# Kernel optimization log

Hardware: AMD Instinct MI355X
Metric: run time of the kernel (lower is better)

The kernel has to match this reference:

```python
import jax, jax.numpy as jnp
import numpy as np

DIM = 1024
NUM_HEADS = 16
HEAD_DIM = DIM // NUM_HEADS
SCALE = HEAD_DIM ** -0.5
CAUSAL = True


def setup_inputs() -> dict:
    key = jax.random.key(0)
    k_x, k_qkv, k_proj, k_pb = jax.random.split(key, 4)
    B, S = 4, 2048
    x = jax.random.normal(k_x, (B, S, DIM), dtype=jnp.float32)
    # nn.Linear(dim, 3*dim, bias=False): weight [3*dim, dim]; store transposed [dim, 3*dim]
    w_qkv = jax.random.normal(k_qkv, (DIM, 3 * DIM), dtype=jnp.float32) * (DIM ** -0.5)
    w_proj = jax.random.normal(k_proj, (DIM, DIM), dtype=jnp.float32) * (DIM ** -0.5)
    b_proj = jax.random.normal(k_pb, (DIM,), dtype=jnp.float32) * 0.01
    return {"x": x, "w_qkv": w_qkv, "w_proj": w_proj, "b_proj": b_proj}


def reference(x, w_qkv, w_proj, b_proj):
    B, S, C = x.shape
    # qkv: [B, S, 3, H, D] -> q,k,v each [B, H, S, D]
    qkv = (x @ w_qkv).reshape(B, S, 3, NUM_HEADS, HEAD_DIM)
    qkv = jnp.transpose(qkv, (2, 0, 3, 1, 4))
    q, k, v = qkv[0], qkv[1], qkv[2]
    # scores [B, H, S, S]
    attn = jnp.einsum('bhqd,bhkd->bhqk', q, k) * SCALE
    if CAUSAL:
        causal_mask = jnp.triu(jnp.ones((S, S), dtype=bool), k=1)
        attn = jnp.where(causal_mask, -jnp.inf, attn)
    attn = jax.nn.softmax(attn, axis=-1)
    out = jnp.einsum('bhqk,bhkd->bhqd', attn, v)
    out = jnp.transpose(out, (0, 2, 1, 3)).reshape(B, S, C)
    return out @ w_proj + b_proj
```

## Files before the change

kernel.cpp:

```cpp
#include <hip/hip_runtime.h>
#include <hip/hip_bf16.h>
#include <math.h>

#define DIMC 1024
#define NHEADS 16
#define HDIM 64
#define BATCH 4
#define SEQ 2048
#define NROWS (BATCH * SEQ)
#define ATTN_SCALE 0.125f
#define LOG2E 1.4426950408889634f

typedef __attribute__((ext_vector_type(8))) short short8;
typedef __attribute__((ext_vector_type(4))) short short4v;
typedef __attribute__((ext_vector_type(4))) float f32x4;

static __device__ __forceinline__ short f2bf(float f) {
    __hip_bfloat16 h = __float2bfloat16(f);
    return *reinterpret_cast<short*>(&h);
}

static __device__ __forceinline__ void gload16(const void* g, void* l) {
    __builtin_amdgcn_global_load_lds(
        (const __attribute__((address_space(1))) unsigned int*)g,
        (__attribute__((address_space(3))) unsigned int*)l, 16, 0, 0);
}

__global__ __launch_bounds__(256)
void xcvt(const float* __restrict__ in, unsigned short* __restrict__ out) {
    int i = blockIdx.x * 256 + threadIdx.x;
    const float4* p = reinterpret_cast<const float4*>(in) + 2 * i;
    float4 a = p[0], b = p[1];
    short8 pk;
    pk[0] = f2bf(a.x); pk[1] = f2bf(a.y); pk[2] = f2bf(a.z); pk[3] = f2bf(a.w);
    pk[4] = f2bf(b.x); pk[5] = f2bf(b.y); pk[6] = f2bf(b.z); pk[7] = f2bf(b.w);
    reinterpret_cast<short8*>(out)[i] = pk;
}

__global__ __launch_bounds__(256)
void transpose_cvt(const float* __restrict__ src, unsigned short* __restrict__ dst,
                   int N) {
    __shared__ float t[64][65];
    const int tid = threadIdx.x;
    const int cb = blockIdx.x * 64;
    const int rb = blockIdx.y * 64;
#pragma unroll
    for (int e = 0; e < 4; e++) {
        int idx = tid + e * 256;
        int row = idx >> 4;
        int c4 = (idx & 15) << 2;
        *reinterpret_cast<float4*>(&t[row][c4]) =
            *reinterpret_cast<const float4*>(&src[(size_t)(rb + row) * N + cb + c4]);
    }
    __syncthreads();
#pragma unroll
    for (int e = 0; e < 2; e++) {
        int idx = tid + e * 256;
        int col = idx >> 3;
        int k8 = (idx & 7) << 3;
        short8 pk;
#pragma unroll
        for (int j = 0; j < 8; j++) pk[j] = f2bf(t[k8 + j][col]);
        *reinterpret_cast<short8*>(&dst[(size_t)(cb + col) * 1024 + rb + k8]) = pk;
    }
}

__global__ __launch_bounds__(256)
void qkv_gemm_mfma(const unsigned short* __restrict__ Xbf,
                   const unsigned short* __restrict__ Wt,
                   unsigned short* __restrict__ qo, unsigned short* __restrict__ ko,
                   unsigned short* __restrict__ vt) {
    __shared__ short Alds[128][32];
    __shared__ short Blds[128][32];
    const int tid = threadIdx.x;
    const int lane = tid & 63;
    const int wave = tid >> 6;
    const int wr = wave >> 1, wc = wave & 1;
    const int rowbase = blockIdx.y * 128;
    const int colbase = blockIdx.x * 128;
    const int g = lane >> 4, li = lane & 15;
    const int srow0 = (wave * 2 + 0) * 16 + (lane >> 2);
    const int srow1 = (wave * 2 + 1) * 16 + (lane >> 2);
    const int scol = (lane & 3) * 8;
    short* aflat = &Alds[0][0];
    short* bflat = &Blds[0][0];

    f32x4 acc[4][4];
#pragma unroll
    for (int m = 0; m < 4; m++)
#pragma unroll
        for (int n = 0; n < 4; n++) acc[m][n] = (f32x4){0.f, 0.f, 0.f, 0.f};

    for (int k0 = 0; k0 < DIMC; k0 += 32) {
        gload16(&Xbf[(size_t)(rowbase + srow0) * DIMC + k0 + scol],
                aflat + (wave * 2 + 0) * 512);
        gload16(&Xbf[(size_t)(rowbase + srow1) * DIMC + k0 + scol],
                aflat + (wave * 2 + 1) * 512);
        gload16(&Wt[(size_t)(colbase + srow0) * 1024 + k0 + scol],
                bflat + (wave * 2 + 0) * 512);
        gload16(&Wt[(size_t)(colbase + srow1) * 1024 + k0 + scol],
                bflat + (wave * 2 + 1) * 512);
        __syncthreads();
        short8 af[4], bfr[4];
#pragma unroll
        for (int m = 0; m < 4; m++)
            af[m] = *reinterpret_cast<const short8*>(&Alds[wr * 64 + m * 16 + li][g * 8]);
#pragma unroll
        for (int n = 0; n < 4; n++)
            bfr[n] = *reinterpret_cast<const short8*>(&Blds[wc * 64 + n * 16 + li][g * 8]);
#pragma unroll
        for (int m = 0; m < 4; m++)
#pragma unroll
            for (int n = 0; n < 4; n++)
                acc[m][n] = __builtin_amdgcn_mfma_f32_16x16x32_bf16(
                    af[m], bfr[n], acc[m][n], 0, 0, 0);
        __syncthreads();
    }

    const int col0 = colbase + wc * 64;
    const int three = col0 >> 10;
    const int h = (col0 & 1023) >> 6;
    if (three < 2) {
        unsigned short* dst = (three == 0) ? qo : ko;
        const float mult = (three == 0) ? (ATTN_SCALE * LOG2E) : 1.0f;
#pragma unroll
        for (int n = 0; n < 4; n++) {
            int d = n * 16 + li;
#pragma unroll
            for (int m = 0; m < 4; m++) {
                int r0 = rowbase + wr * 64 + m * 16 + g * 4;
                int b = r0 >> 11;
                size_t base = ((size_t)(b * NHEADS + h) * SEQ) * HDIM + d;
#pragma unroll
                for (int r = 0; r < 4; r++) {
                    int s = (r0 + r) & 2047;
                    dst[base + (size_t)s * HDIM] = (unsigned short)f2bf(acc[m][n][r] * mult);
                }
            }
        }
    } else {
#pragma unroll
        for (int n = 0; n < 4; n++) {
            int d = n * 16 + li;
#pragma unroll
            for (int m = 0; m < 4; m++) {
                int r0 = rowbase + wr * 64 + m * 16 + g * 4;
                int b = r0 >> 11, s0 = r0 & 2047;
                short4v pk;
#pragma unroll
                for (int r = 0; r < 4; r++) pk[r] = f2bf(acc[m][n][r]);
                *reinterpret_cast<short4v*>(
                    &vt[((size_t)(b * NHEADS + h) * HDIM + d) * SEQ + s0]) = pk;
            }
        }
    }
}

__global__ __launch_bounds__(256)
void proj_gemm_mfma(const unsigned short* __restrict__ Abf,
                    const unsigned short* __restrict__ Wt,
                    const float* __restrict__ bias, float* __restrict__ out) {
    __shared__ short Alds[128][32];
    __shared__ short Blds[128][32];
    const int tid = threadIdx.x;
    const int lane = tid & 63;
    const int wave = tid >> 6;
    const int wr = wave >> 1, wc = wave & 1;
    const int rowbase = blockIdx.y * 128;
    const int colbase = blockIdx.x * 128;
    const int g = lane >> 4, li = lane & 15;
    const int srow0 = (wave * 2 + 0) * 16 + (lane >> 2);
    const int srow1 = (wave * 2 + 1) * 16 + (lane >> 2);
    const int scol = (lane & 3) * 8;
    short* aflat = &Alds[0][0];
    short* bflat = &Blds[0][0];

    f32x4 acc[4][4];
#pragma unroll
    for (int m = 0; m < 4; m++)
#pragma unroll
        for (int n = 0; n < 4; n++) acc[m][n] = (f32x4){0.f, 0.f, 0.f, 0.f};

    for (int k0 = 0; k0 < DIMC; k0 += 32) {
        gload16(&Abf[(size_t)(rowbase + srow0) * DIMC + k0 + scol],
                aflat + (wave * 2 + 0) * 512);
        gload16(&Abf[(size_t)(rowbase + srow1) * DIMC + k0 + scol],
                aflat + (wave * 2 + 1) * 512);
        gload16(&Wt[(size_t)(colbase + srow0) * 1024 + k0 + scol],
                bflat + (wave * 2 + 0) * 512);
        gload16(&Wt[(size_t)(colbase + srow1) * 1024 + k0 + scol],
                bflat + (wave * 2 + 1) * 512);
        __syncthreads();
        short8 af[4], bfr[4];
#pragma unroll
        for (int m = 0; m < 4; m++)
            af[m] = *reinterpret_cast<const short8*>(&Alds[wr * 64 + m * 16 + li][g * 8]);
#pragma unroll
        for (int n = 0; n < 4; n++)
            bfr[n] = *reinterpret_cast<const short8*>(&Blds[wc * 64 + n * 16 + li][g * 8]);
#pragma unroll
        for (int m = 0; m < 4; m++)
#pragma unroll
            for (int n = 0; n < 4; n++)
                acc[m][n] = __builtin_amdgcn_mfma_f32_16x16x32_bf16(
                    af[m], bfr[n], acc[m][n], 0, 0, 0);
        __syncthreads();
    }

#pragma unroll
    for (int n = 0; n < 4; n++) {
        int col = colbase + wc * 64 + n * 16 + li;
        float bv = bias[col];
#pragma unroll
        for (int m = 0; m < 4; m++) {
            int r0 = rowbase + wr * 64 + m * 16 + g * 4;
#pragma unroll
            for (int r = 0; r < 4; r++)
                out[(size_t)(r0 + r) * DIMC + col] = acc[m][n][r] + bv;
        }
    }
}

__global__ __launch_bounds__(256)
void flash_attn_mfma(const unsigned short* __restrict__ qg,
                     const unsigned short* __restrict__ kg,
                     const unsigned short* __restrict__ vt,
                     unsigned short* __restrict__ og) {
    __shared__ short Klds[2][64][64];
    __shared__ short Vlds[2][64][64];
    __shared__ short Plds[4][32][64];
    const int tid = threadIdx.x;
    const int lane = tid & 63;
    const int w = tid >> 6;
    const int g = lane >> 4, li = lane & 15;
    const int sw = li & 7;
    const int orig = blockIdx.x;
    const int swz = (orig & 7) * 128 + (orig >> 3);
    const int bh = swz >> 4;
    const int qtile = 15 - (swz & 15);
    const size_t head = (size_t)bh * SEQ * HDIM;
    const int b = bh >> 4, h = bh & 15;

    const int c0r = tid >> 3, c0c = tid & 7;

    const int qbase = qtile * 128;
    const int qw = qbase + w * 32;
    const int nt = 2 * qtile + 2;

    short8 bq[2][2];
#pragma unroll
    for (int n = 0; n < 2; n++)
#pragma unroll
        for (int ds = 0; ds < 2; ds++)
            bq[n][ds] = *reinterpret_cast<const short8*>(
                &qg[head + (size_t)(qw + li + 16 * n) * HDIM + ds * 32 + g * 8]);

    f32x4 accO[4][2];
#pragma unroll
    for (int df = 0; df < 4; df++)
#pragma unroll
        for (int n = 0; n < 2; n++) accO[df][n] = (f32x4){0.f, 0.f, 0.f, 0.f};
    float mrow[2] = {-INFINITY, -INFINITY};
    float lrow[2] = {0.f, 0.f};

    const unsigned short* kp = kg + head + (size_t)c0r * HDIM + c0c * 8;
    const unsigned short* vp = vt + head + (size_t)c0r * SEQ + c0c * 8;

    short8 kreg0, kreg1, vreg0, vreg1;
    kreg0 = *reinterpret_cast<const short8*>(kp);
    kreg1 = *reinterpret_cast<const short8*>(kp + 32 * HDIM);
    vreg0 = *reinterpret_cast<const short8*>(vp);
    vreg1 = *reinterpret_cast<const short8*>(vp + 32 * SEQ);
    kp += 64 * HDIM; vp += 64;
    {
        const int sw0 = (c0c ^ (c0r & 7)) * 8;
        const int sw1 = (c0c ^ ((c0r + 32) & 7)) * 8;
        *reinterpret_cast<short8*>(&Klds[0][c0r][sw0]) = kreg0;
        *reinterpret_cast<short8*>(&Vlds[0][c0r][sw0]) = vreg0;
        *reinterpret_cast<short8*>(&Klds[0][c0r + 32][sw1]) = kreg1;
        *reinterpret_cast<short8*>(&Vlds[0][c0r + 32][sw1]) = vreg1;
    }
    __syncthreads();

    for (int t = 0; t < nt; t++) {
        const int kvbase = t * 64;
        const int buf = t & 1;
        const bool more = (t + 1 < nt);
        if (more) {
            kreg0 = *reinterpret_cast<const short8*>(kp);
            kreg1 = *reinterpret_cast<const short8*>(kp + 32 * HDIM);
            vreg0 = *reinterpret_cast<const short8*>(vp);
            vreg1 = *reinterpret_cast<const short8*>(vp + 32 * SEQ);
            kp += 64 * HDIM; vp += 64;
        }

        if (kvbase <= qw + 31) {
            f32x4 s[4][2];
#pragma unroll
            for (int m = 0; m < 4; m++)
#pragma unroll
                for (int n = 0; n < 2; n++) s[m][n] = (f32x4){0.f, 0.f, 0.f, 0.f};
#pragma unroll
            for (int ds = 0; ds < 2; ds++) {
                short8 ak[4];
#pragma unroll
                for (int m = 0; m < 4; m++)
                    ak[m] = *reinterpret_cast<const short8*>(
                        &Klds[buf][li + 16 * m][(((ds * 4 + g) ^ sw)) * 8]);
#pragma unroll
                for (int m = 0; m < 4; m++)
#pragma unroll
                    for (int n = 0; n < 2; n++)
                        s[m][n] = __builtin_amdgcn_mfma_f32_16x16x32_bf16(
                            ak[m], bq[n][ds], s[m][n], 0, 0, 0);
            }
            const bool diag = (kvbase + 63 > qw);
            if (diag) {
#pragma unroll
                for (int n = 0; n < 2; n++) {
                    int q = qw + li + 16 * n;
#pragma unroll
                    for (int m = 0; m < 4; m++)
#pragma unroll
                        for (int r = 0; r < 4; r++) {
                            int kv = kvbase + 16 * m + 4 * g + r;
                            if (kv > q) s[m][n][r] = -INFINITY;
                        }
                }
            }
            float corr[2];
#pragma unroll
            for (int n = 0; n < 2; n++) {
                float a0 = fmaxf(fmaxf(s[0][n][0], s[0][n][1]), fmaxf(s[0][n][2], s[0][n][3]));
                float a1 = fmaxf(fmaxf(s[1][n][0], s[1][n][1]), fmaxf(s[1][n][2], s[1][n][3]));
                float a2 = fmaxf(fmaxf(s[2][n][0], s[2][n][1]), fmaxf(s[2][n][2], s[2][n][3]));
                float a3 = fmaxf(fmaxf(s[3][n][0], s[3][n][1]), fmaxf(s[3][n][2], s[3][n][3]));
                float tm = fmaxf(fmaxf(a0, a1), fmaxf(a2, a3));
                tm = fmaxf(tm, __shfl_xor(tm, 16));
                tm = fmaxf(tm, __shfl_xor(tm, 32));
                float mnew = fmaxf(mrow[n], tm);
                corr[n] = __builtin_amdgcn_exp2f(mrow[n] - mnew);
                mrow[n] = mnew;
            }
            float sm[4][2];
#pragma unroll
            for (int m = 0; m < 4; m++) {
#pragma unroll
                for (int n = 0; n < 2; n++) {
                    float p0 = __builtin_amdgcn_exp2f(s[m][n][0] - mrow[n]);
                    float p1 = __builtin_amdgcn_exp2f(s[m][n][1] - mrow[n]);
                    float p2 = __builtin_amdgcn_exp2f(s[m][n][2] - mrow[n]);
                    float p3 = __builtin_amdgcn_exp2f(s[m][n][3] - mrow[n]);
                    sm[m][n] = (p0 + p1) + (p2 + p3);
                    unsigned u01 = (__float_as_uint(p1) & 0xFFFF0000u) |
                                   (__float_as_uint(p0) >> 16);
                    unsigned u23 = (__float_as_uint(p3) & 0xFFFF0000u) |
                                   (__float_as_uint(p2) >> 16);
                    *reinterpret_cast<uint2*>(
                        &Plds[w][li + 16 * n]
                             [((2 * m + (g >> 1)) ^ sw) * 8 + (g & 1) * 4]) =
                        make_uint2(u01, u23);
                }
            }
#pragma unroll
            for (int n = 0; n < 2; n++) {
                float ts = (sm[0][n] + sm[1][n]) + (sm[2][n] + sm[3][n]);
                ts += __shfl_xor(ts, 16);
                ts += __shfl_xor(ts, 32);
                lrow[n] = lrow[n] * corr[n] + ts;
            }
            bool nore = (corr[0] == 1.0f) && (corr[1] == 1.0f);
            if (!__all((int)nore)) {
#pragma unroll
                for (int df = 0; df < 4; df++)
#pragma unroll
                    for (int n = 0; n < 2; n++) {
                        accO[df][n][0] *= corr[n]; accO[df][n][1] *= corr[n];
                        accO[df][n][2] *= corr[n]; accO[df][n][3] *= corr[n];
                    }
            }
#pragma unroll
            for (int ks = 0; ks < 2; ks++) {
                short8 av[4], bp[2];
#pragma unroll
                for (int df = 0; df < 4; df++)
                    av[df] = *reinterpret_cast<const short8*>(
                        &Vlds[buf][li + 16 * df][((ks * 4 + g) ^ sw) * 8]);
#pragma unroll
                for (int n = 0; n < 2; n++)
                    bp[n] = *reinterpret_cast<const short8*>(
                        &Plds[w][li + 16 * n][((ks * 4 + g) ^ sw) * 8]);
#pragma unroll
                for (int df = 0; df < 4; df++)
#pragma unroll
                    for (int n = 0; n < 2; n++)
                        accO[df][n] = __builtin_amdgcn_mfma_f32_16x16x32_bf16(
                            av[df], bp[n], accO[df][n], 0, 0, 0);
            }
        }

        if (more) {
            const int nbuf = buf ^ 1;
            const int sw0 = (c0c ^ (c0r & 7)) * 8;
            const int sw1 = (c0c ^ ((c0r + 32) & 7)) * 8;
            *reinterpret_cast<short8*>(&Klds[nbuf][c0r][sw0]) = kreg0;
            *reinterpret_cast<short8*>(&Vlds[nbuf][c0r][sw0]) = vreg0;
            *reinterpret_cast<short8*>(&Klds[nbuf][c0r + 32][sw1]) = kreg1;
            *reinterpret_cast<short8*>(&Vlds[nbuf][c0r + 32][sw1]) = vreg1;
        }
        __syncthreads();
    }

#pragma unroll
    for (int n = 0; n < 2; n++) {
        float inv = 1.0f / lrow[n];
        int q = qw + li + 16 * n;
        size_t rowoff = (size_t)(b * SEQ + q) * DIMC + h * HDIM;
#pragma unroll
        for (int df = 0; df < 4; df++) {
            short4v pk;
#pragma unroll
            for (int r = 0; r < 4; r++) pk[r] = f2bf(accO[df][n][r] * inv);
            *reinterpret_cast<short4v*>(&og[rowoff + 16 * df + 4 * g]) = pk;
        }
    }
}

extern "C" void kernel_launch(void* const* d_in, const int* in_sizes, int n_in,
                              void* d_out, int out_size, void* d_ws, size_t ws_size,
                              hipStream_t stream) {
    const float* x      = (const float*)d_in[0];
    const float* w_qkv  = (const float*)d_in[1];
    const float* w_proj = (const float*)d_in[2];
    const float* b_proj = (const float*)d_in[3];
    float* out = (float*)d_out;

    char* w = (char*)d_ws;
    unsigned short* qb  = (unsigned short*)(w);
    unsigned short* kb  = (unsigned short*)(w + ((size_t)16 << 20));
    unsigned short* vtb = (unsigned short*)(w + ((size_t)32 << 20));
    unsigned short* ao  = (unsigned short*)(w + ((size_t)48 << 20));
    unsigned short* wqt = (unsigned short*)(w + ((size_t)64 << 20));
    unsigned short* wpt = (unsigned short*)(w + ((size_t)72 << 20));
    unsigned short* xbf = (unsigned short*)(w + ((size_t)80 << 20));

    xcvt<<<NROWS * DIMC / (256 * 8), 256, 0, stream>>>(x, xbf);
    transpose_cvt<<<dim3(3 * DIMC / 64, DIMC / 64), 256, 0, stream>>>(w_qkv, wqt, 3 * DIMC);
    transpose_cvt<<<dim3(DIMC / 64, DIMC / 64), 256, 0, stream>>>(w_proj, wpt, DIMC);
    qkv_gemm_mfma<<<dim3(3 * DIMC / 128, NROWS / 128), 256, 0, stream>>>(xbf, wqt, qb, kb, vtb);
    flash_attn_mfma<<<1024, 256, 0, stream>>>(qb, kb, vtb, ao);
    proj_gemm_mfma<<<dim3(DIMC / 128, NROWS / 128), 256, 0, stream>>>(ao, wpt, b_proj, out);
}
```

Measured before the change: 299.6 us.

## Pair causal q-tiles per attention block and double GEMM K-step to 64

The flash-attention kernel now launches half as many blocks, and each block handles two q-tiles (bx and 15-bx) of one head in sequence. This balances the causal triangular workload so every block does the same total number of KV tiles. Separately, both GEMMs load 64-wide K slices per iteration and issue two MFMA substeps per barrier pair, which halves the number of synchronizations. The cost is doubled LDS per GEMM block, and fewer attention blocks, which may reduce occupancy and latency hiding.

Measured after the change: 279.7 us. 1.07x faster.

```diff
diff --git a/kernel.cpp b/kernel.cpp
--- a/kernel.cpp
+++ b/kernel.cpp
@@ -70,8 +70,8 @@
                    const unsigned short* __restrict__ Wt,
                    unsigned short* __restrict__ qo, unsigned short* __restrict__ ko,
                    unsigned short* __restrict__ vt) {
-    __shared__ short Alds[128][32];
-    __shared__ short Blds[128][32];
+    __shared__ short Alds[128][64];
+    __shared__ short Blds[128][64];
     const int tid = threadIdx.x;
     const int lane = tid & 63;
     const int wave = tid >> 6;
@@ -79,9 +79,8 @@
     const int rowbase = blockIdx.y * 128;
     const int colbase = blockIdx.x * 128;
     const int g = lane >> 4, li = lane & 15;
-    const int srow0 = (wave * 2 + 0) * 16 + (lane >> 2);
-    const int srow1 = (wave * 2 + 1) * 16 + (lane >> 2);
-    const int scol = (lane & 3) * 8;
+    const int sr = lane >> 3;
+    const int sc = (lane & 7) * 8;
     short* aflat = &Alds[0][0];
     short* bflat = &Blds[0][0];
 
@@ -91,29 +90,34 @@
 #pragma unroll
         for (int n = 0; n < 4; n++) acc[m][n] = (f32x4){0.f, 0.f, 0.f, 0.f};
 
-    for (int k0 = 0; k0 < DIMC; k0 += 32) {
-        gload16(&Xbf[(size_t)(rowbase + srow0) * DIMC + k0 + scol],
-                aflat + (wave * 2 + 0) * 512);
-        gload16(&Xbf[(size_t)(rowbase + srow1) * DIMC + k0 + scol],
-                aflat + (wave * 2 + 1) * 512);
-        gload16(&Wt[(size_t)(colbase + srow0) * 1024 + k0 + scol],
-                bflat + (wave * 2 + 0) * 512);
-        gload16(&Wt[(size_t)(colbase + srow1) * 1024 + k0 + scol],
-                bflat + (wave * 2 + 1) * 512);
-        __syncthreads();
-        short8 af[4], bfr[4];
-#pragma unroll
-        for (int m = 0; m < 4; m++)
-            af[m] = *reinterpret_cast<const short8*>(&Alds[wr * 64 + m * 16 + li][g * 8]);
-#pragma unroll
-        for (int n = 0; n < 4; n++)
-            bfr[n] = *reinterpret_cast<const short8*>(&Blds[wc * 64 + n * 16 + li][g * 8]);
-#pragma unroll
-        for (int m = 0; m < 4; m++)
+    for (int k0 = 0; k0 < DIMC; k0 += 64) {
+#pragma unroll
+        for (int e = 0; e < 4; e++) {
+            int j = wave * 4 + e;
+            gload16(&Xbf[(size_t)(rowbase + j * 8 + sr) * DIMC + k0 + sc],
+                    aflat + j * 512);
+            gload16(&Wt[(size_t)(colbase + j * 8 + sr) * 1024 + k0 + sc],
+                    bflat + j * 512);
+        }
+        __syncthreads();
+#pragma unroll
+        for (int ks = 0; ks < 2; ks++) {
+            short8 af[4], bfr[4];
+#pragma unroll
+            for (int m = 0; m < 4; m++)
+                af[m] = *reinterpret_cast<const short8*>(
+                    &Alds[wr * 64 + m * 16 + li][ks * 32 + g * 8]);
 #pragma unroll
             for (int n = 0; n < 4; n++)
-                acc[m][n] = __builtin_amdgcn_mfma_f32_16x16x32_bf16(
-                    af[m], bfr[n], acc[m][n], 0, 0, 0);
+                bfr[n] = *reinterpret_cast<const short8*>(
+                    &Blds[wc * 64 + n * 16 + li][ks * 32 + g * 8]);
+#pragma unroll
+            for (int m = 0; m < 4; m++)
+#pragma unroll
+                for (int n = 0; n < 4; n++)
+                    acc[m][n] = __builtin_amdgcn_mfma_f32_16x16x32_bf16(
+                        af[m], bfr[n], acc[m][n], 0, 0, 0);
+        }
         __syncthreads();
     }
 
@@ -160,8 +164,8 @@
 void proj_gemm_mfma(const unsigned short* __restrict__ Abf,
                     const unsigned short* __restrict__ Wt,
                     const float* __restrict__ bias, float* __restrict__ out) {
-    __shared__ short Alds[128][32];
-    __shared__ short Blds[128][32];
+    __shared__ short Alds[128][64];
+    __shared__ short Blds[128][64];
     const int tid = threadIdx.x;
     const int lane = tid & 63;
     const int wave = tid >> 6;
@@ -169,9 +173,8 @@
     const int rowbase = blockIdx.y * 128;
     const int colbase = blockIdx.x * 128;
     const int g = lane >> 4, li = lane & 15;
-    const int srow0 = (wave * 2 + 0) * 16 + (lane >> 2);
-    const int srow1 = (wave * 2 + 1) * 16 + (lane >> 2);
-    const int scol = (lane & 3) * 8;
+    const int sr = lane >> 3;
+    const int sc = (lane & 7) * 8;
     short* aflat = &Alds[0][0];
     short* bflat = &Blds[0][0];
 
@@ -181,29 +184,34 @@
 #pragma unroll
         for (int n = 0; n < 4; n++) acc[m][n] = (f32x4){0.f, 0.f, 0.f, 0.f};
 
-    for (int k0 = 0; k0 < DIMC; k0 += 32) {
-        gload16(&Abf[(size_t)(rowbase + srow0) * DIMC + k0 + scol],
-                aflat + (wave * 2 + 0) * 512);
-        gload16(&Abf[(size_t)(rowbase + srow1) * DIMC + k0 + scol],
-                aflat + (wave * 2 + 1) * 512);
-        gload16(&Wt[(size_t)(colbase + srow0) * 1024 + k0 + scol],
-                bflat + (wave * 2 + 0) * 512);
-        gload16(&Wt[(size_t)(colbase + srow1) * 1024 + k0 + scol],
-                bflat + (wave * 2 + 1) * 512);
-        __syncthreads();
-        short8 af[4], bfr[4];
-#pragma unroll
-        for (int m = 0; m < 4; m++)
-            af[m] = *reinterpret_cast<const short8*>(&Alds[wr * 64 + m * 16 + li][g * 8]);
-#pragma unroll
-        for (int n = 0; n < 4; n++)
-            bfr[n] = *reinterpret_cast<const short8*>(&Blds[wc * 64 + n * 16 + li][g * 8]);
-#pragma unroll
-        for (int m = 0; m < 4; m++)
+    for (int k0 = 0; k0 < DIMC; k0 += 64) {
+#pragma unroll
+        for (int e = 0; e < 4; e++) {
+            int j = wave * 4 + e;
+            gload16(&Abf[(size_t)(rowbase + j * 8 + sr) * DIMC + k0 + sc],
+                    aflat + j * 512);
+            gload16(&Wt[(size_t)(colbase + j * 8 + sr) * 1024 + k0 + sc],
+                    bflat + j * 512);
+        }
+        __syncthreads();
+#pragma unroll
+        for (int ks = 0; ks < 2; ks++) {
+            short8 af[4], bfr[4];
+#pragma unroll
+            for (int m = 0; m < 4; m++)
+                af[m] = *reinterpret_cast<const short8*>(
+                    &Alds[wr * 64 + m * 16 + li][ks * 32 + g * 8]);
 #pragma unroll
             for (int n = 0; n < 4; n++)
-                acc[m][n] = __builtin_amdgcn_mfma_f32_16x16x32_bf16(
-                    af[m], bfr[n], acc[m][n], 0, 0, 0);
+                bfr[n] = *reinterpret_cast<const short8*>(
+                    &Blds[wc * 64 + n * 16 + li][ks * 32 + g * 8]);
+#pragma unroll
+            for (int m = 0; m < 4; m++)
+#pragma unroll
+                for (int n = 0; n < 4; n++)
+                    acc[m][n] = __builtin_amdgcn_mfma_f32_16x16x32_bf16(
+                        af[m], bfr[n], acc[m][n], 0, 0, 0);
+        }
         __syncthreads();
     }
 
@@ -235,194 +243,198 @@
     const int g = lane >> 4, li = lane & 15;
     const int sw = li & 7;
     const int orig = blockIdx.x;
-    const int swz = (orig & 7) * 128 + (orig >> 3);
-    const int bh = swz >> 4;
-    const int qtile = 15 - (swz & 15);
+    const int swz = (orig & 7) * 64 + (orig >> 3);
+    const int bx = swz & 7;
+    const int bh = swz >> 3;
     const size_t head = (size_t)bh * SEQ * HDIM;
     const int b = bh >> 4, h = bh & 15;
 
     const int c0r = tid >> 3, c0c = tid & 7;
 
-    const int qbase = qtile * 128;
-    const int qw = qbase + w * 32;
-    const int nt = 2 * qtile + 2;
-
-    short8 bq[2][2];
-#pragma unroll
-    for (int n = 0; n < 2; n++)
-#pragma unroll
-        for (int ds = 0; ds < 2; ds++)
-            bq[n][ds] = *reinterpret_cast<const short8*>(
-                &qg[head + (size_t)(qw + li + 16 * n) * HDIM + ds * 32 + g * 8]);
-
-    f32x4 accO[4][2];
-#pragma unroll
-    for (int df = 0; df < 4; df++)
-#pragma unroll
-        for (int n = 0; n < 2; n++) accO[df][n] = (f32x4){0.f, 0.f, 0.f, 0.f};
-    float mrow[2] = {-INFINITY, -INFINITY};
-    float lrow[2] = {0.f, 0.f};
-
-    const unsigned short* kp = kg + head + (size_t)c0r * HDIM + c0c * 8;
-    const unsigned short* vp = vt + head + (size_t)c0r * SEQ + c0c * 8;
-
-    short8 kreg0, kreg1, vreg0, vreg1;
-    kreg0 = *reinterpret_cast<const short8*>(kp);
-    kreg1 = *reinterpret_cast<const short8*>(kp + 32 * HDIM);
-    vreg0 = *reinterpret_cast<const short8*>(vp);
-    vreg1 = *reinterpret_cast<const short8*>(vp + 32 * SEQ);
-    kp += 64 * HDIM; vp += 64;
-    {
-        const int sw0 = (c0c ^ (c0r & 7)) * 8;
-        const int sw1 = (c0c ^ ((c0r + 32) & 7)) * 8;
-        *reinterpret_cast<short8*>(&Klds[0][c0r][sw0]) = kreg0;
-        *reinterpret_cast<short8*>(&Vlds[0][c0r][sw0]) = vreg0;
-        *reinterpret_cast<short8*>(&Klds[0][c0r + 32][sw1]) = kreg1;
-        *reinterpret_cast<short8*>(&Vlds[0][c0r + 32][sw1]) = vreg1;
-    }
-    __syncthreads();
-
-    for (int t = 0; t < nt; t++) {
-        const int kvbase = t * 64;
-        const int buf = t & 1;
-        const bool more = (t + 1 < nt);
-        if (more) {
-            kreg0 = *reinterpret_cast<const short8*>(kp);
-            kreg1 = *reinterpret_cast<const short8*>(kp + 32 * HDIM);
-            vreg0 = *reinterpret_cast<const short8*>(vp);
-            vreg1 = *reinterpret_cast<const short8*>(vp + 32 * SEQ);
-            kp += 64 * HDIM; vp += 64;
-        }
-
-        if (kvbase <= qw + 31) {
-            f32x4 s[4][2];
-#pragma unroll
-            for (int m = 0; m < 4; m++)
-#pragma unroll
-                for (int n = 0; n < 2; n++) s[m][n] = (f32x4){0.f, 0.f, 0.f, 0.f};
-#pragma unroll
-            for (int ds = 0; ds < 2; ds++) {
-                short8 ak[4];
-#pragma unroll
-                for (int m = 0; m < 4; m++)
-                    ak[m] = *reinterpret_cast<const short8*>(
-                        &Klds[buf][li + 16 * m][(((ds * 4 + g) ^ sw)) * 8]);
-#pragma unroll
-                for (int m = 0; m < 4; m++)
-#pragma unroll
-                    for (int n = 0; n < 2; n++)
-                        s[m][n] = __builtin_amdgcn_mfma_f32_16x16x32_bf16(
-                            ak[m], bq[n][ds], s[m][n], 0, 0, 0);
-            }
-            const bool diag = (kvbase + 63 > qw);
-            if (diag) {
-#pragma unroll
-                for (int n = 0; n < 2; n++) {
-                    int q = qw + li + 16 * n;
-#pragma unroll
-                    for (int m = 0; m < 4; m++)
-#pragma unroll
-                        for (int r = 0; r < 4; r++) {
-                            int kv = kvbase + 16 * m + 4 * g + r;
-                            if (kv > q) s[m][n][r] = -INFINITY;
-                        }
-                }
-            }
-            float corr[2];
-#pragma unroll
-            for (int n = 0; n < 2; n++) {
-                float a0 = fmaxf(fmaxf(s[0][n][0], s[0][n][1]), fmaxf(s[0][n][2], s[0][n][3]));
-                float a1 = fmaxf(fmaxf(s[1][n][0], s[1][n][1]), fmaxf(s[1][n][2], s[1][n][3]));
-                float a2 = fmaxf(fmaxf(s[2][n][0], s[2][n][1]), fmaxf(s[2][n][2], s[2][n][3]));
-                float a3 = fmaxf(fmaxf(s[3][n][0], s[3][n][1]), fmaxf(s[3][n][2], s[3][n][3]));
-                float tm = fmaxf(fmaxf(a0, a1), fmaxf(a2, a3));
-                tm = fmaxf(tm, __shfl_xor(tm, 16));
-                tm = fmaxf(tm, __shfl_xor(tm, 32));
-                float mnew = fmaxf(mrow[n], tm);
-                corr[n] = __builtin_amdgcn_exp2f(mrow[n] - mnew);
-                mrow[n] = mnew;
-            }
-            float sm[4][2];
-#pragma unroll
-            for (int m = 0; m < 4; m++) {
-#pragma unroll
-                for (int n = 0; n < 2; n++) {
-                    float p0 = __builtin_amdgcn_exp2f(s[m][n][0] - mrow[n]);
-                    float p1 = __builtin_amdgcn_exp2f(s[m][n][1] - mrow[n]);
-                    float p2 = __builtin_amdgcn_exp2f(s[m][n][2] - mrow[n]);
-                    float p3 = __builtin_amdgcn_exp2f(s[m][n][3] - mrow[n]);
-                    sm[m][n] = (p0 + p1) + (p2 + p3);
-                    unsigned u01 = (__float_as_uint(p1) & 0xFFFF0000u) |
-                                   (__float_as_uint(p0) >> 16);
-                    unsigned u23 = (__float_as_uint(p3) & 0xFFFF0000u) |
-                                   (__float_as_uint(p2) >> 16);
-                    *reinterpret_cast<uint2*>(
-                        &Plds[w][li + 16 * n]
-                             [((2 * m + (g >> 1)) ^ sw) * 8 + (g & 1) * 4]) =
-                        make_uint2(u01, u23);
-                }
-            }
-#pragma unroll
-            for (int n = 0; n < 2; n++) {
-                float ts = (sm[0][n] + sm[1][n]) + (sm[2][n] + sm[3][n]);
-                ts += __shfl_xor(ts, 16);
-                ts += __shfl_xor(ts, 32);
-                lrow[n] = lrow[n] * corr[n] + ts;
-            }
-            bool nore = (corr[0] == 1.0f) && (corr[1] == 1.0f);
-            if (!__all((int)nore)) {
-#pragma unroll
-                for (int df = 0; df < 4; df++)
-#pragma unroll
-                    for (int n = 0; n < 2; n++) {
-                        accO[df][n][0] *= corr[n]; accO[df][n][1] *= corr[n];
-                        accO[df][n][2] *= corr[n]; accO[df][n][3] *= corr[n];
-                    }
-            }
-#pragma unroll
-            for (int ks = 0; ks < 2; ks++) {
-                short8 av[4], bp[2];
-#pragma unroll
-                for (int df = 0; df < 4; df++)
-                    av[df] = *reinterpret_cast<const short8*>(
-                        &Vlds[buf][li + 16 * df][((ks * 4 + g) ^ sw) * 8]);
-#pragma unroll
-                for (int n = 0; n < 2; n++)
-                    bp[n] = *reinterpret_cast<const short8*>(
-                        &Plds[w][li + 16 * n][((ks * 4 + g) ^ sw) * 8]);
-#pragma unroll
-                for (int df = 0; df < 4; df++)
-#pragma unroll
-                    for (int n = 0; n < 2; n++)
-                        accO[df][n] = __builtin_amdgcn_mfma_f32_16x16x32_bf16(
-                            av[df], bp[n], accO[df][n], 0, 0, 0);
-            }
-        }
-
-        if (more) {
-            const int nbuf = buf ^ 1;
+    for (int pass = 0; pass < 2; pass++) {
+        const int qtile = pass ? (15 - bx) : bx;
+        const int qbase = qtile * 128;
+        const int qw = qbase + w * 32;
+        const int nt = 2 * qtile + 2;
+
+        short8 bq[2][2];
+#pragma unroll
+        for (int n = 0; n < 2; n++)
+#pragma unroll
+            for (int ds = 0; ds < 2; ds++)
+                bq[n][ds] = *reinterpret_cast<const short8*>(
+                    &qg[head + (size_t)(qw + li + 16 * n) * HDIM + ds * 32 + g * 8]);
+
+        f32x4 accO[4][2];
+#pragma unroll
+        for (int df = 0; df < 4; df++)
+#pragma unroll
+            for (int n = 0; n < 2; n++) accO[df][n] = (f32x4){0.f, 0.f, 0.f, 0.f};
+        float mrow[2] = {-INFINITY, -INFINITY};
+        float lrow[2] = {0.f, 0.f};
+
+        const unsigned short* kp = kg + head + (size_t)c0r * HDIM + c0c * 8;
+        const unsigned short* vp = vt + head + (size_t)c0r * SEQ + c0c * 8;
+
+        short8 kreg0, kreg1, vreg0, vreg1;
+        kreg0 = *reinterpret_cast<const short8*>(kp);
+        kreg1 = *reinterpret_cast<const short8*>(kp + 32 * HDIM);
+        vreg0 = *reinterpret_cast<const short8*>(vp);
+        vreg1 = *reinterpret_cast<const short8*>(vp + 32 * SEQ);
+        kp += 64 * HDIM; vp += 64;
+        {
             const int sw0 = (c0c ^ (c0r & 7)) * 8;
             const int sw1 = (c0c ^ ((c0r + 32) & 7)) * 8;
-            *reinterpret_cast<short8*>(&Klds[nbuf][c0r][sw0]) = kreg0;
-            *reinterpret_cast<short8*>(&Vlds[nbuf][c0r][sw0]) = vreg0;
-            *reinterpret_cast<short8*>(&Klds[nbuf][c0r + 32][sw1]) = kreg1;
-            *reinterpret_cast<short8*>(&Vlds[nbuf][c0r + 32][sw1]) = vreg1;
-        }
-        __syncthreads();
-    }
-
-#pragma unroll
-    for (int n = 0; n < 2; n++) {
-        float inv = 1.0f / lrow[n];
-        int q = qw + li + 16 * n;
-        size_t rowoff = (size_t)(b * SEQ + q) * DIMC + h * HDIM;
-#pragma unroll
-        for (int df = 0; df < 4; df++) {
-            short4v pk;
-#pragma unroll
-            for (int r = 0; r < 4; r++) pk[r] = f2bf(accO[df][n][r] * inv);
-            *reinterpret_cast<short4v*>(&og[rowoff + 16 * df + 4 * g]) = pk;
-        }
+            *reinterpret_cast<short8*>(&Klds[0][c0r][sw0]) = kreg0;
+            *reinterpret_cast<short8*>(&Vlds[0][c0r][sw0]) = vreg0;
+            *reinterpret_cast<short8*>(&Klds[0][c0r + 32][sw1]) = kreg1;
+            *reinterpret_cast<short8*>(&Vlds[0][c0r + 32][sw1]) = vreg1;
+        }
+        __syncthreads();
+
+        for (int t = 0; t < nt; t++) {
+            const int kvbase = t * 64;
+            const int buf = t & 1;
+            const bool more = (t + 1 < nt);
+            if (more) {
+                kreg0 = *reinterpret_cast<const short8*>(kp);
+                kreg1 = *reinterpret_cast<const short8*>(kp + 32 * HDIM);
+                vreg0 = *reinterpret_cast<const short8*>(vp);
+                vreg1 = *reinterpret_cast<const short8*>(vp + 32 * SEQ);
+                kp += 64 * HDIM; vp += 64;
+            }
+
+            if (kvbase <= qw + 31) {
+                f32x4 s[4][2];
+#pragma unroll
+                for (int m = 0; m < 4; m++)
+#pragma unroll
+                    for (int n = 0; n < 2; n++) s[m][n] = (f32x4){0.f, 0.f, 0.f, 0.f};
+#pragma unroll
+                for (int ds = 0; ds < 2; ds++) {
+                    short8 ak[4];
+#pragma unroll
+                    for (int m = 0; m < 4; m++)
+                        ak[m] = *reinterpret_cast<const short8*>(
+                            &Klds[buf][li + 16 * m][(((ds * 4 + g) ^ sw)) * 8]);
+#pragma unroll
+                    for (int m = 0; m < 4; m++)
+#pragma unroll
+                        for (int n = 0; n < 2; n++)
+                            s[m][n] = __builtin_amdgcn_mfma_f32_16x16x32_bf16(
+                                ak[m], bq[n][ds], s[m][n], 0, 0, 0);
+                }
+                const bool diag = (kvbase + 63 > qw);
+                if (diag) {
+#pragma unroll
+                    for (int n = 0; n < 2; n++) {
+                        int q = qw + li + 16 * n;
+#pragma unroll
+                        for (int m = 0; m < 4; m++)
+#pragma unroll
+                            for (int r = 0; r < 4; r++) {
+                                int kv = kvbase + 16 * m + 4 * g + r;
+                                if (kv > q) s[m][n][r] = -INFINITY;
+                            }
+                    }
+                }
+                float corr[2];
+#pragma unroll
+                for (int n = 0; n < 2; n++) {
+                    float a0 = fmaxf(fmaxf(s[0][n][0], s[0][n][1]), fmaxf(s[0][n][2], s[0][n][3]));
+                    float a1 = fmaxf(fmaxf(s[1][n][0], s[1][n][1]), fmaxf(s[1][n][2], s[1][n][3]));
+                    float a2 = fmaxf(fmaxf(s[2][n][0], s[2][n][1]), fmaxf(s[2][n][2], s[2][n][3]));
+                    float a3 = fmaxf(fmaxf(s[3][n][0], s[3][n][1]), fmaxf(s[3][n][2], s[3][n][3]));
+                    float tm = fmaxf(fmaxf(a0, a1), fmaxf(a2, a3));
+                    tm = fmaxf(tm, __shfl_xor(tm, 16));
+                    tm = fmaxf(tm, __shfl_xor(tm, 32));
+                    float mnew = fmaxf(mrow[n], tm);
+                    corr[n] = __builtin_amdgcn_exp2f(mrow[n] - mnew);
+                    mrow[n] = mnew;
+                }
+                float sm[4][2];
+#pragma unroll
+                for (int m = 0; m < 4; m++) {
+#pragma unroll
+                    for (int n = 0; n < 2; n++) {
+                        float p0 = __builtin_amdgcn_exp2f(s[m][n][0] - mrow[n]);
+                        float p1 = __builtin_amdgcn_exp2f(s[m][n][1] - mrow[n]);
+                        float p2 = __builtin_amdgcn_exp2f(s[m][n][2] - mrow[n]);
+                        float p3 = __builtin_amdgcn_exp2f(s[m][n][3] - mrow[n]);
+                        sm[m][n] = (p0 + p1) + (p2 + p3);
+                        unsigned u01 = (__float_as_uint(p1) & 0xFFFF0000u) |
+                                       (__float_as_uint(p0) >> 16);
+                        unsigned u23 = (__float_as_uint(p3) & 0xFFFF0000u) |
+                                       (__float_as_uint(p2) >> 16);
+                        *reinterpret_cast<uint2*>(
+                            &Plds[w][li + 16 * n]
+                                 [((2 * m + (g >> 1)) ^ sw) * 8 + (g & 1) * 4]) =
+                            make_uint2(u01, u23);
+                    }
+                }
+#pragma unroll
+                for (int n = 0; n < 2; n++) {
+                    float ts = (sm[0][n] + sm[1][n]) + (sm[2][n] + sm[3][n]);
+                    ts += __shfl_xor(ts, 16);
+                    ts += __shfl_xor(ts, 32);
+                    lrow[n] = lrow[n] * corr[n] + ts;
+                }
+                bool nore = (corr[0] == 1.0f) && (corr[1] == 1.0f);
+                if (!__all((int)nore)) {
+#pragma unroll
+                    for (int df = 0; df < 4; df++)
+#pragma unroll
+                        for (int n = 0; n < 2; n++) {
+                            accO[df][n][0] *= corr[n]; accO[df][n][1] *= corr[n];
+                            accO[df][n][2] *= corr[n]; accO[df][n][3] *= corr[n];
+                        }
+                }
+#pragma unroll
+                for (int ks = 0; ks < 2; ks++) {
+                    short8 av[4], bp[2];
+#pragma unroll
+                    for (int df = 0; df < 4; df++)
+                        av[df] = *reinterpret_cast<const short8*>(
+                            &Vlds[buf][li + 16 * df][((ks * 4 + g) ^ sw) * 8]);
+#pragma unroll
+                    for (int n = 0; n < 2; n++)
+                        bp[n] = *reinterpret_cast<const short8*>(
+                            &Plds[w][li + 16 * n][((ks * 4 + g) ^ sw) * 8]);
+#pragma unroll
+                    for (int df = 0; df < 4; df++)
+#pragma unroll
+                        for (int n = 0; n < 2; n++)
+                            accO[df][n] = __builtin_amdgcn_mfma_f32_16x16x32_bf16(
+                                av[df], bp[n], accO[df][n], 0, 0, 0);
+                }
+            }
+
+            if (more) {
+                const int nbuf = buf ^ 1;
+                const int sw0 = (c0c ^ (c0r & 7)) * 8;
+                const int sw1 = (c0c ^ ((c0r + 32) & 7)) * 8;
+                *reinterpret_cast<short8*>(&Klds[nbuf][c0r][sw0]) = kreg0;
+                *reinterpret_cast<short8*>(&Vlds[nbuf][c0r][sw0]) = vreg0;
+                *reinterpret_cast<short8*>(&Klds[nbuf][c0r + 32][sw1]) = kreg1;
+                *reinterpret_cast<short8*>(&Vlds[nbuf][c0r + 32][sw1]) = vreg1;
+            }
+            __syncthreads();
+        }
+
+#pragma unroll
+        for (int n = 0; n < 2; n++) {
+            float inv = 1.0f / lrow[n];
+            int q = qw + li + 16 * n;
+            size_t rowoff = (size_t)(b * SEQ + q) * DIMC + h * HDIM;
+#pragma unroll
+            for (int df = 0; df < 4; df++) {
+                short4v pk;
+#pragma unroll
+                for (int r = 0; r < 4; r++) pk[r] = f2bf(accO[df][n][r] * inv);
+                *reinterpret_cast<short4v*>(&og[rowoff + 16 * df + 4 * g]) = pk;
+            }
+        }
+        __syncthreads();
     }
 }
 
@@ -448,6 +460,6 @@
     transpose_cvt<<<dim3(3 * DIMC / 64, DIMC / 64), 256, 0, stream>>>(w_qkv, wqt, 3 * DIMC);
     transpose_cvt<<<dim3(DIMC / 64, DIMC / 64), 256, 0, stream>>>(w_proj, wpt, DIMC);
     qkv_gemm_mfma<<<dim3(3 * DIMC / 128, NROWS / 128), 256, 0, stream>>>(xbf, wqt, qb, kb, vtb);
-    flash_attn_mfma<<<1024, 256, 0, stream>>>(qb, kb, vtb, ao);
+    flash_attn_mfma<<<512, 256, 0, stream>>>(qb, kb, vtb, ao);
     proj_gemm_mfma<<<dim3(DIMC / 128, NROWS / 128), 256, 0, stream>>>(ao, wpt, b_proj, out);
 }
```
